# Kernel tuning notes

Hardware: AMD Instinct MI355X
Metric: run time of the kernel (lower is better)

Reference implementation:

```python
import jax, jax.numpy as jnp
import numpy as np

B, T, D = 4096, 200, 64
H = 32  # hidden units of score MLP
NEG_INF = jnp.float32(-2**32 + 1)


def setup_inputs() -> dict:
    key = jax.random.key(0)
    k1, k2, k3, k4, k5 = jax.random.split(key, 5)
    query = jax.random.normal(k1, (B, 1, D), dtype=jnp.float32)
    keys = jax.random.normal(k2, (B, T, D), dtype=jnp.float32)
    mask = jax.random.randint(k3, (B, T), 0, 2) > 0
    mask = mask.at[:, 0].set(True)  # ensure at least one valid key per row
    # Glorot-normal-ish init for the tiny score MLP
    W1 = jax.random.normal(k4, (3 * D, H), dtype=jnp.float32) * jnp.sqrt(2.0 / (3 * D + H))
    b1 = jnp.zeros((H,), dtype=jnp.float32)
    W2 = jax.random.normal(k5, (H, 1), dtype=jnp.float32) * jnp.sqrt(2.0 / (H + 1))
    b2 = jnp.zeros((1,), dtype=jnp.float32)
    return {"query": query, "keys": keys, "mask": mask,
            "W1": W1, "b1": b1, "W2": W2, "b2": b2}


def reference(query, keys, mask, W1, b1, W2, b2):
    b, t, d = keys.shape
    q = jnp.broadcast_to(query, (b, t, d))            # tile query over seq
    att_in = jnp.concatenate([q, keys, q - keys], axis=-1)   # [B,T,3D]
    h = jax.nn.sigmoid(att_in @ W1 + b1)              # [B,T,H]
    score = (h @ W2 + b2)[..., 0]                     # [B,T]
    score = jnp.where(mask, score, NEG_INF)
    w = jax.nn.softmax(score, axis=-1)                # [B,T]
    out = jnp.einsum('bt,btd->bd', w, keys)           # weighted key sum
    return out[:, None, :]                            # [B,1,D]
```

## Files before the change

### kernel.cpp

```cpp
#include <hip/hip_runtime.h>
#include <hip/hip_bf16.h>


#define B 4096
#define T 200
#define D 64
#define H 32
#define TP 208
#define KP 72

typedef __attribute__((ext_vector_type(8))) short short8;
typedef __attribute__((ext_vector_type(4))) float f32x4;


__global__ __launch_bounds__(256) void prep_kernel(
        const float* __restrict__ W1,
        const float* __restrict__ b1,
        const float* __restrict__ query,
        float*       __restrict__ qa_ws,
        unsigned short* __restrict__ wkf)
{
    int blk = blockIdx.x;
    int n = blk * 256 + threadIdx.x;
    if (blk < (B * H) / 256) {
        int b = n >> 5;
        int j = n & 31;
        const float* qb = query + (size_t)b * D;
        float acc = b1[j];
        #pragma unroll 8
        for (int i = 0; i < D; ++i)
            acc = fmaf(qb[i], W1[i * H + j] + W1[(128 + i) * H + j], acc);
        qa_ws[n] = acc;
    } else {
        int m = n - (B * H);
        int e  = m & 7;
        int l  = (m >> 3) & 63;
        int fs = m >> 9;
        int ntile = fs >> 1, kstep = fs & 1;
        int k = kstep * 32 + (l >> 4) * 8 + e;
        int j = ntile * 16 + (l & 15);
        float v = W1[(64 + k) * H + j] - W1[(128 + k) * H + j];
        __hip_bfloat16 hv = __float2bfloat16(v);
        wkf[m] = __builtin_bit_cast(unsigned short, hv);
    }
}

__global__ __launch_bounds__(256, 5) void attn_pool_kernel(
        const float* __restrict__ keys,
        const int*   __restrict__ mask,
        const unsigned short* __restrict__ wkf,
        const float* __restrict__ qa_all,
        const float* __restrict__ W2,
        float*       __restrict__ out)
{
    __shared__ unsigned short kt[TP * KP];
    __shared__ float sc_lds[TP];
    __shared__ float red[8];

    const int tid  = threadIdx.x;
    const int b    = blockIdx.x;
    const int wv   = tid >> 6;
    const int lane = tid & 63;
    const int quad = lane >> 4;
    const int l15  = lane & 15;

    const float4* kp = reinterpret_cast<const float4*>(keys + (size_t)b * (T * D));
    for (int idx = tid; idx < (T * D) / 4; idx += 256) {
        float4 v = kp[idx];
        int t  = idx >> 4;
        int i4 = idx & 15;
        __hip_bfloat16 h0 = __float2bfloat16(v.x);
        __hip_bfloat16 h1 = __float2bfloat16(v.y);
        __hip_bfloat16 h2 = __float2bfloat16(v.z);
        __hip_bfloat16 h3 = __float2bfloat16(v.w);
        ushort4 u;
        u.x = __builtin_bit_cast(unsigned short, h0);
        u.y = __builtin_bit_cast(unsigned short, h1);
        u.z = __builtin_bit_cast(unsigned short, h2);
        u.w = __builtin_bit_cast(unsigned short, h3);
        *reinterpret_cast<ushort4*>(&kt[t * KP + i4 * 4]) = u;
    }
    if (tid < 144) {
        ushort4 z; z.x = z.y = z.z = z.w = 0;
        *reinterpret_cast<ushort4*>(&kt[T * KP + tid * 4]) = z;
    }

    const short8* wf = reinterpret_cast<const short8*>(wkf);
    short8 bfrag[4];
    #pragma unroll
    for (int fs = 0; fs < 4; ++fs)
        bfrag[fs] = wf[fs * 64 + lane];

    const float* qa = qa_all + (size_t)b * H;
    float qa0 = qa[l15];
    float qa1 = qa[16 + l15];
    float w20 = W2[l15];
    float w21 = W2[16 + l15];

    __syncthreads();

    for (int m0 = wv; m0 < TP / 16; m0 += 4) {
        const int trow = m0 * 16 + l15;
        short8 a0 = *reinterpret_cast<const short8*>(&kt[trow * KP + quad * 8]);
        short8 a1 = *reinterpret_cast<const short8*>(&kt[trow * KP + 32 + quad * 8]);

        f32x4 acc0 = {0.f, 0.f, 0.f, 0.f};
        f32x4 acc1 = {0.f, 0.f, 0.f, 0.f};
        acc0 = __builtin_amdgcn_mfma_f32_16x16x32_bf16(a0, bfrag[0], acc0, 0, 0, 0);
        acc0 = __builtin_amdgcn_mfma_f32_16x16x32_bf16(a1, bfrag[1], acc0, 0, 0, 0);
        acc1 = __builtin_amdgcn_mfma_f32_16x16x32_bf16(a0, bfrag[2], acc1, 0, 0, 0);
        acc1 = __builtin_amdgcn_mfma_f32_16x16x32_bf16(a1, bfrag[3], acc1, 0, 0, 0);

        #pragma unroll
        for (int r = 0; r < 4; ++r) {
            float x0 = acc0[r] + qa0;
            float x1 = acc1[r] + qa1;
            float s0 = __builtin_amdgcn_rcpf(1.0f + exp2f(-x0 * 1.44269504088896340736f));
            float s1 = __builtin_amdgcn_rcpf(1.0f + exp2f(-x1 * 1.44269504088896340736f));
            float p = fmaf(s0, w20, s1 * w21);
            #pragma unroll
            for (int off = 1; off <= 8; off <<= 1)
                p += __shfl_xor(p, off, 64);
            if (l15 == 0)
                sc_lds[m0 * 16 + quad * 4 + r] = p;
        }
    }
    __syncthreads();

    const int t = tid;
    float s = (t < T) ? ((mask[(size_t)b * T + t] != 0) ? sc_lds[t] : -4294967295.0f)
                      : -INFINITY;

    float m = s;
    #pragma unroll
    for (int off = 32; off >= 1; off >>= 1)
        m = fmaxf(m, __shfl_xor(m, off, 64));
    if (lane == 0) red[wv] = m;
    __syncthreads();
    m = fmaxf(fmaxf(red[0], red[1]), fmaxf(red[2], red[3]));

    float e = (t < T) ? exp2f((s - m) * 1.44269504088896340736f) : 0.0f;
    float tot = e;
    #pragma unroll
    for (int off = 32; off >= 1; off >>= 1)
        tot += __shfl_xor(tot, off, 64);
    if (lane == 0) red[4 + wv] = tot;
    __syncthreads();
    tot = (red[4] + red[5]) + (red[6] + red[7]);

    if (t < T) sc_lds[t] = e * __builtin_amdgcn_rcpf(tot);
    __syncthreads();

    float* part = reinterpret_cast<float*>(kt);
    {
        const float* krow = keys + (size_t)b * (T * D);
        float acc = 0.0f;
        const int t0 = wv * 50;
        #pragma unroll 5
        for (int tt = t0; tt < t0 + 50; ++tt)
            acc = fmaf(sc_lds[tt], krow[tt * D + lane], acc);
        part[wv * 64 + lane] = acc;
    }
    __syncthreads();
    if (tid < 64) {
        out[(size_t)b * D + tid] =
            ((part[tid] + part[64 + tid]) + (part[128 + tid] + part[192 + tid]));
    }
}

extern "C" void kernel_launch(void* const* d_in, const int* in_sizes, int n_in,
                              void* d_out, int out_size, void* d_ws, size_t ws_size,
                              hipStream_t stream) {
    const float* query = (const float*)d_in[0];
    const float* keys  = (const float*)d_in[1];
    const int*   mask  = (const int*)d_in[2];
    const float* W1    = (const float*)d_in[3];
    const float* b1    = (const float*)d_in[4];
    const float* W2    = (const float*)d_in[5];

    float* qa = (float*)d_ws;
    unsigned short* wkf = (unsigned short*)(qa + B * H);

    prep_kernel<<<(B * H) / 256 + 8, 256, 0, stream>>>(W1, b1, query, qa, wkf);
    attn_pool_kernel<<<B, 256, 0, stream>>>(keys, mask, wkf, qa, W2, (float*)d_out);
}
```

Baseline: 335.9 us.

## Fuse score MLP, softmax and weighted sum into one pass over keys

```diff
diff --git a/kernel.cpp b/kernel.cpp
--- a/kernel.cpp
+++ b/kernel.cpp
@@ -6,8 +6,8 @@
 #define T 200
 #define D 64
 #define H 32
-#define TP 208
-#define KP 72
+#define LOG2E 1.44269504088896340736f
+#define SOFF 16.0f
 
 typedef __attribute__((ext_vector_type(8))) short short8;
 typedef __attribute__((ext_vector_type(4))) float f32x4;
@@ -45,6 +45,11 @@
     }
 }
 
+__device__ __forceinline__ unsigned short bf16u(float x) {
+    __hip_bfloat16 h = __float2bfloat16(x);
+    return __builtin_bit_cast(unsigned short, h);
+}
+
 __global__ __launch_bounds__(256, 5) void attn_pool_kernel(
         const float* __restrict__ keys,
         const int*   __restrict__ mask,
@@ -53,9 +58,8 @@
         const float* __restrict__ W2,
         float*       __restrict__ out)
 {
-    __shared__ unsigned short kt[TP * KP];
-    __shared__ float sc_lds[TP];
-    __shared__ float red[8];
+    __shared__ float part[4][64];
+    __shared__ float denw[4];
 
     const int tid  = threadIdx.x;
     const int b    = blockIdx.x;
@@ -64,107 +68,113 @@
     const int quad = lane >> 4;
     const int l15  = lane & 15;
 
-    const float4* kp = reinterpret_cast<const float4*>(keys + (size_t)b * (T * D));
-    for (int idx = tid; idx < (T * D) / 4; idx += 256) {
-        float4 v = kp[idx];
-        int t  = idx >> 4;
-        int i4 = idx & 15;
-        __hip_bfloat16 h0 = __float2bfloat16(v.x);
-        __hip_bfloat16 h1 = __float2bfloat16(v.y);
-        __hip_bfloat16 h2 = __float2bfloat16(v.z);
-        __hip_bfloat16 h3 = __float2bfloat16(v.w);
-        ushort4 u;
-        u.x = __builtin_bit_cast(unsigned short, h0);
-        u.y = __builtin_bit_cast(unsigned short, h1);
-        u.z = __builtin_bit_cast(unsigned short, h2);
-        u.w = __builtin_bit_cast(unsigned short, h3);
-        *reinterpret_cast<ushort4*>(&kt[t * KP + i4 * 4]) = u;
-    }
-    if (tid < 144) {
-        ushort4 z; z.x = z.y = z.z = z.w = 0;
-        *reinterpret_cast<ushort4*>(&kt[T * KP + tid * 4]) = z;
+    const short8* wf = reinterpret_cast<const short8*>(wkf);
+    short8 bf0 = wf[0 * 64 + lane];
+    short8 bf1 = wf[1 * 64 + lane];
+    short8 bf2 = wf[2 * 64 + lane];
+    short8 bf3 = wf[3 * 64 + lane];
+
+    const float* qa = qa_all + (size_t)b * H;
+    const float qa0 = qa[l15];
+    const float qa1 = qa[16 + l15];
+    const float w20 = W2[l15];
+    const float w21 = W2[16 + l15];
+
+    const float4* krow = reinterpret_cast<const float4*>(keys + (size_t)b * (T * D));
+    const int*    mrow = mask + (size_t)b * T;
+
+    float acc[16];
+    #pragma unroll
+    for (int e = 0; e < 16; ++e) acc[e] = 0.0f;
+    float den = 0.0f;
+
+    for (int m0 = wv; m0 < 13; m0 += 4) {
+        const int t  = m0 * 16 + l15;
+        const int tr = (t < T) ? t : (T - 1);
+
+        float4 k0 = krow[tr * 16 + quad * 2 + 0];
+        float4 k1 = krow[tr * 16 + quad * 2 + 1];
+        float4 k2 = krow[tr * 16 + 8 + quad * 2 + 0];
+        float4 k3 = krow[tr * 16 + 8 + quad * 2 + 1];
+        int mval = mrow[tr];
+
+        short8 a0, a1;
+        a0[0] = (short)bf16u(k0.x); a0[1] = (short)bf16u(k0.y);
+        a0[2] = (short)bf16u(k0.z); a0[3] = (short)bf16u(k0.w);
+        a0[4] = (short)bf16u(k1.x); a0[5] = (short)bf16u(k1.y);
+        a0[6] = (short)bf16u(k1.z); a0[7] = (short)bf16u(k1.w);
+        a1[0] = (short)bf16u(k2.x); a1[1] = (short)bf16u(k2.y);
+        a1[2] = (short)bf16u(k2.z); a1[3] = (short)bf16u(k2.w);
+        a1[4] = (short)bf16u(k3.x); a1[5] = (short)bf16u(k3.y);
+        a1[6] = (short)bf16u(k3.z); a1[7] = (short)bf16u(k3.w);
+
+        f32x4 c0 = {0.f, 0.f, 0.f, 0.f};
+        f32x4 c1 = {0.f, 0.f, 0.f, 0.f};
+        c0 = __builtin_amdgcn_mfma_f32_16x16x32_bf16(a0, bf0, c0, 0, 0, 0);
+        c0 = __builtin_amdgcn_mfma_f32_16x16x32_bf16(a1, bf1, c0, 0, 0, 0);
+        c1 = __builtin_amdgcn_mfma_f32_16x16x32_bf16(a0, bf2, c1, 0, 0, 0);
+        c1 = __builtin_amdgcn_mfma_f32_16x16x32_bf16(a1, bf3, c1, 0, 0, 0);
+
+        float p[4];
+        #pragma unroll
+        for (int r = 0; r < 4; ++r) {
+            float x0 = c0[r] + qa0;
+            float x1 = c1[r] + qa1;
+            float s0 = __builtin_amdgcn_rcpf(1.0f + exp2f(-x0 * LOG2E));
+            float s1 = __builtin_amdgcn_rcpf(1.0f + exp2f(-x1 * LOG2E));
+            p[r] = fmaf(s0, w20, s1 * w21);
+        }
+        #pragma unroll
+        for (int r = 0; r < 4; ++r) {
+            #pragma unroll
+            for (int off = 1; off <= 8; off <<= 1)
+                p[r] += __shfl_xor(p[r], off, 64);
+        }
+        const int addr = (l15 >> 2) << 6;
+        int q0 = __builtin_amdgcn_ds_bpermute(addr, __builtin_bit_cast(int, p[0]));
+        int q1 = __builtin_amdgcn_ds_bpermute(addr, __builtin_bit_cast(int, p[1]));
+        int q2 = __builtin_amdgcn_ds_bpermute(addr, __builtin_bit_cast(int, p[2]));
+        int q3 = __builtin_amdgcn_ds_bpermute(addr, __builtin_bit_cast(int, p[3]));
+        const int rsel = l15 & 3;
+        int s01 = (rsel & 1) ? q1 : q0;
+        int s23 = (rsel & 1) ? q3 : q2;
+        float st = __builtin_bit_cast(float, (rsel & 2) ? s23 : s01);
+
+        float w = ((t < T) && (mval != 0)) ? exp2f((st - SOFF) * LOG2E) : 0.0f;
+        den += w;
+
+        acc[0]  = fmaf(w, k0.x, acc[0]);  acc[1]  = fmaf(w, k0.y, acc[1]);
+        acc[2]  = fmaf(w, k0.z, acc[2]);  acc[3]  = fmaf(w, k0.w, acc[3]);
+        acc[4]  = fmaf(w, k1.x, acc[4]);  acc[5]  = fmaf(w, k1.y, acc[5]);
+        acc[6]  = fmaf(w, k1.z, acc[6]);  acc[7]  = fmaf(w, k1.w, acc[7]);
+        acc[8]  = fmaf(w, k2.x, acc[8]);  acc[9]  = fmaf(w, k2.y, acc[9]);
+        acc[10] = fmaf(w, k2.z, acc[10]); acc[11] = fmaf(w, k2.w, acc[11]);
+        acc[12] = fmaf(w, k3.x, acc[12]); acc[13] = fmaf(w, k3.y, acc[13]);
+        acc[14] = fmaf(w, k3.z, acc[14]); acc[15] = fmaf(w, k3.w, acc[15]);
     }
 
-    const short8* wf = reinterpret_cast<const short8*>(wkf);
-    short8 bfrag[4];
     #pragma unroll
-    for (int fs = 0; fs < 4; ++fs)
-        bfrag[fs] = wf[fs * 64 + lane];
+    for (int off = 1; off <= 8; off <<= 1) {
+        #pragma unroll
+        for (int e = 0; e < 16; ++e)
+            acc[e] += __shfl_xor(acc[e], off, 64);
+        den += __shfl_xor(den, off, 64);
+    }
 
-    const float* qa = qa_all + (size_t)b * H;
-    float qa0 = qa[l15];
-    float qa1 = qa[16 + l15];
-    float w20 = W2[l15];
-    float w21 = W2[16 + l15];
-
-    __syncthreads();
-
-    for (int m0 = wv; m0 < TP / 16; m0 += 4) {
-        const int trow = m0 * 16 + l15;
-        short8 a0 = *reinterpret_cast<const short8*>(&kt[trow * KP + quad * 8]);
-        short8 a1 = *reinterpret_cast<const short8*>(&kt[trow * KP + 32 + quad * 8]);
-
-        f32x4 acc0 = {0.f, 0.f, 0.f, 0.f};
-        f32x4 acc1 = {0.f, 0.f, 0.f, 0.f};
-        acc0 = __builtin_amdgcn_mfma_f32_16x16x32_bf16(a0, bfrag[0], acc0, 0, 0, 0);
-        acc0 = __builtin_amdgcn_mfma_f32_16x16x32_bf16(a1, bfrag[1], acc0, 0, 0, 0);
-        acc1 = __builtin_amdgcn_mfma_f32_16x16x32_bf16(a0, bfrag[2], acc1, 0, 0, 0);
-        acc1 = __builtin_amdgcn_mfma_f32_16x16x32_bf16(a1, bfrag[3], acc1, 0, 0, 0);
-
+    if (l15 == 0) {
         #pragma unroll
-        for (int r = 0; r < 4; ++r) {
-            float x0 = acc0[r] + qa0;
-            float x1 = acc1[r] + qa1;
-            float s0 = __builtin_amdgcn_rcpf(1.0f + exp2f(-x0 * 1.44269504088896340736f));
-            float s1 = __builtin_amdgcn_rcpf(1.0f + exp2f(-x1 * 1.44269504088896340736f));
-            float p = fmaf(s0, w20, s1 * w21);
-            #pragma unroll
-            for (int off = 1; off <= 8; off <<= 1)
-                p += __shfl_xor(p, off, 64);
-            if (l15 == 0)
-                sc_lds[m0 * 16 + quad * 4 + r] = p;
+        for (int e = 0; e < 8; ++e) {
+            part[wv][quad * 8 + e]      = acc[e];
+            part[wv][32 + quad * 8 + e] = acc[8 + e];
         }
+        if (quad == 0) denw[wv] = den;
     }
     __syncthreads();
 
-    const int t = tid;
-    float s = (t < T) ? ((mask[(size_t)b * T + t] != 0) ? sc_lds[t] : -4294967295.0f)
-                      : -INFINITY;
-
-    float m = s;
-    #pragma unroll
-    for (int off = 32; off >= 1; off >>= 1)
-        m = fmaxf(m, __shfl_xor(m, off, 64));
-    if (lane == 0) red[wv] = m;
-    __syncthreads();
-    m = fmaxf(fmaxf(red[0], red[1]), fmaxf(red[2], red[3]));
-
-    float e = (t < T) ? exp2f((s - m) * 1.44269504088896340736f) : 0.0f;
-    float tot = e;
-    #pragma unroll
-    for (int off = 32; off >= 1; off >>= 1)
-        tot += __shfl_xor(tot, off, 64);
-    if (lane == 0) red[4 + wv] = tot;
-    __syncthreads();
-    tot = (red[4] + red[5]) + (red[6] + red[7]);
-
-    if (t < T) sc_lds[t] = e * __builtin_amdgcn_rcpf(tot);
-    __syncthreads();
-
-    float* part = reinterpret_cast<float*>(kt);
-    {
-        const float* krow = keys + (size_t)b * (T * D);
-        float acc = 0.0f;
-        const int t0 = wv * 50;
-        #pragma unroll 5
-        for (int tt = t0; tt < t0 + 50; ++tt)
-            acc = fmaf(sc_lds[tt], krow[tt * D + lane], acc);
-        part[wv * 64 + lane] = acc;
-    }
-    __syncthreads();
     if (tid < 64) {
-        out[(size_t)b * D + tid] =
-            ((part[tid] + part[64 + tid]) + (part[128 + tid] + part[192 + tid]));
+        float dtot = (denw[0] + denw[1]) + (denw[2] + denw[3]);
+        float v = (part[0][tid] + part[1][tid]) + (part[2][tid] + part[3][tid]);
+        out[(size_t)b * D + tid] = v * __builtin_amdgcn_rcpf(dtot);
     }
 }
 
```

Result: faster. 305.1 us (-9.2%).
